# Kernel tuning notes

Hardware: AMD Instinct MI355X
Metric: run time of the kernel (lower is better)

## Reference

```python
import jax, jax.numpy as jnp
import numpy as np

HIDDEN = 1024
HEADS = 16
HEAD_D = HIDDEN // HEADS
FILL = -10000.0


def setup_inputs() -> dict:
    key = jax.random.key(0)
    ks = jax.random.split(key, 5)
    scale = 1.0 / np.sqrt(HIDDEN)
    x = jax.random.normal(ks[0], (2, 2048, HIDDEN), dtype=jnp.float32)
    # nn.Linear weights stored as [in, out] (already transposed vs torch)
    W_qkv = jax.random.uniform(ks[1], (HIDDEN, 3 * HIDDEN), dtype=jnp.float32, minval=-scale, maxval=scale)
    b_qkv = jax.random.uniform(ks[2], (3 * HIDDEN,), dtype=jnp.float32, minval=-scale, maxval=scale)
    W_o = jax.random.uniform(ks[3], (HIDDEN, HIDDEN), dtype=jnp.float32, minval=-scale, maxval=scale)
    b_o = jax.random.uniform(ks[4], (HIDDEN,), dtype=jnp.float32, minval=-scale, maxval=scale)
    return {"x": x, "W_qkv": W_qkv, "b_qkv": b_qkv, "W_o": W_o, "b_o": b_o}


def reference(x, W_qkv, b_qkv, W_o, b_o):
    b, s, _ = x.shape
    qkv = x @ W_qkv + b_qkv                       # [b, s, 3*hidden]
    q, k, v = jnp.split(qkv, 3, axis=-1)
    # [b, s, hidden] -> [b, h, s, d]
    def to_heads(t):
        return t.reshape(b, s, HEADS, HEAD_D).transpose(0, 2, 1, 3)
    q, k, v = to_heads(q), to_heads(k), to_heads(v)
    logits = jnp.einsum('bhqd,bhkd->bhqk', q, k) / np.sqrt(HEAD_D).astype(np.float32)
    # Faithful to the original: tril, then fill anything equal to 0 (incl.
    # genuine zeros) with the masked_logit_fill value.
    logits_tril = jnp.tril(logits)
    logits_masked = jnp.where(logits_tril == 0.0, jnp.float32(FILL), logits_tril)
    probs = jax.nn.softmax(logits_masked, axis=-1)
    pre_o = jnp.einsum('bhqk,bhkd->bhqd', probs, v)    # [b, h, s, d]
    pre_o = pre_o.transpose(0, 2, 1, 3).reshape(b, s, HIDDEN)
    return pre_o @ W_o + b_o
```

## Files before the change

### kernel.cpp

```cpp
#include <hip/hip_runtime.h>

typedef __attribute__((ext_vector_type(8))) short short8;
typedef __attribute__((ext_vector_type(4))) short short4b;
typedef __attribute__((ext_vector_type(4))) float f32x4;

static __device__ __forceinline__ short f2bf(float f) {
    unsigned u = __builtin_bit_cast(unsigned, f);
    u += 0x7FFFu + ((u >> 16) & 1u);
    return (short)(u >> 16);
}

static __device__ __forceinline__ void g2l16(const void* g, void* l) {
    __builtin_amdgcn_global_load_lds(
        (const __attribute__((address_space(1))) unsigned*)g,
        (__attribute__((address_space(3))) unsigned*)l, 16, 0, 0);
}

__global__ void convert_x(const float* __restrict__ x, short* __restrict__ xb, int n4) {
    int i = blockIdx.x * blockDim.x + threadIdx.x;
    if (i >= n4) return;
    f32x4 v = *(const f32x4*)&x[(long)i * 4];
    short4b o;
    #pragma unroll
    for (int j = 0; j < 4; ++j) o[j] = f2bf(v[j]);
    *(short4b*)&xb[(long)i * 4] = o;
}

__global__ void transpose_conv(const float* __restrict__ W, short* __restrict__ Wt,
                               int K, int N) {
    __shared__ float lds[64][65];
    const int t = threadIdx.x;
    const int n0 = blockIdx.x * 64, k0 = blockIdx.y * 64;
    const int rr = t >> 4, q4 = (t & 15) * 4;
    #pragma unroll
    for (int p = 0; p < 4; ++p) {
        int k = rr + p * 16;
        f32x4 v = *(const f32x4*)&W[(long)(k0 + k) * N + n0 + q4];
        #pragma unroll
        for (int j = 0; j < 4; ++j) lds[k][q4 + j] = v[j];
    }
    __syncthreads();
    #pragma unroll
    for (int p = 0; p < 4; ++p) {
        int nloc = rr + p * 16;
        short4b o;
        #pragma unroll
        for (int j = 0; j < 4; ++j) o[j] = f2bf(lds[q4 + j][nloc]);
        *(short4b*)&Wt[(long)(n0 + nloc) * K + k0 + q4] = o;
    }
}

template<int F32OUT>
__global__ __launch_bounds__(256, 2)
void gemm_bt(const short* __restrict__ A, const short* __restrict__ Bt,
             const float* __restrict__ bias, void* __restrict__ C,
             int M, int N, int K) {
    __shared__ short lA[128 * 32];
    __shared__ short lB[128 * 32];
    const int t = threadIdx.x;
    const int lane = t & 63, w = t >> 6;
    const int m0 = blockIdx.y * 128, n0 = blockIdx.x * 128;
    const int lr = lane & 15, lk = lane >> 4;
    const int wr = w >> 1, wc = w & 1;

    f32x4 acc[4][4];
    #pragma unroll
    for (int i = 0; i < 4; ++i)
        #pragma unroll
        for (int j = 0; j < 4; ++j)
            #pragma unroll
            for (int e = 0; e < 4; ++e) acc[i][j][e] = 0.0f;

    const int nsteps = K >> 5;
    for (int kt = 0; kt < nsteps; ++kt) {
        const int kb = kt * 32;
        #pragma unroll
        for (int c = 0; c < 2; ++c) {
            int off  = c * 4096 + w * 1024;
            int offl = off + lane * 16;
            int ra = offl >> 6;
            int ca = (offl & 63) >> 1;
            g2l16(A  + (long)(m0 + ra) * K + kb + ca, (short*)lA + (off >> 1));
            g2l16(Bt + (long)(n0 + ra) * K + kb + ca, (short*)lB + (off >> 1));
        }
        __syncthreads();
        short8 af[4], bf[4];
        #pragma unroll
        for (int m = 0; m < 4; ++m)
            af[m] = *(const short8*)&lA[(wr * 64 + m * 16 + lr) * 32 + lk * 8];
        #pragma unroll
        for (int n = 0; n < 4; ++n)
            bf[n] = *(const short8*)&lB[(wc * 64 + n * 16 + lr) * 32 + lk * 8];
        #pragma unroll
        for (int m = 0; m < 4; ++m)
            #pragma unroll
            for (int n = 0; n < 4; ++n)
                acc[m][n] = __builtin_amdgcn_mfma_f32_16x16x32_bf16(af[m], bf[n], acc[m][n], 0, 0, 0);
        __syncthreads();
    }

    #pragma unroll
    for (int n = 0; n < 4; ++n) {
        int col = n0 + wc * 64 + n * 16 + lr;
        float bb = bias[col];
        #pragma unroll
        for (int m = 0; m < 4; ++m) {
            int rowb = m0 + wr * 64 + m * 16 + lk * 4;
            #pragma unroll
            for (int r = 0; r < 4; ++r) {
                float v = acc[m][n][r] + bb;
                if (F32OUT) ((float*)C)[(long)(rowb + r) * N + col] = v;
                else        ((short*)C)[(long)(rowb + r) * N + col] = f2bf(v);
            }
        }
    }
}

__global__ void build_vt(const short* __restrict__ qkv, short* __restrict__ vt) {
    __shared__ short lds[64][72];
    const int t = threadIdx.x;
    const int st = blockIdx.x, bh = blockIdx.y;
    const int b = bh >> 4, h = bh & 15;
    const int s0 = st * 64;
    const int sr = t >> 3, c8 = (t & 7) * 8;
    #pragma unroll
    for (int p = 0; p < 2; ++p) {
        int s = sr + p * 32;
        short8 v = *(const short8*)&qkv[(long)(b * 2048 + s0 + s) * 3072 + 2048 + h * 64 + c8];
        *(short8*)&lds[s][c8] = v;
    }
    __syncthreads();
    #pragma unroll
    for (int p = 0; p < 2; ++p) {
        int d = sr + p * 32;
        short8 v;
        #pragma unroll
        for (int j = 0; j < 8; ++j) v[j] = lds[c8 + j][d];
        *(short8*)&vt[(long)(bh * 64 + d) * 2048 + s0 + c8] = v;
    }
}

__global__ __launch_bounds__(256, 2)
void attn_kernel(const short* __restrict__ qkv, const short* __restrict__ vt,
                 short* __restrict__ pre_o) {
    __shared__ short lK[64 * 64];
    __shared__ short lV[64 * 64];
    __shared__ short lP[4][32 * 64];
    const int t = threadIdx.x, lane = t & 63, w = t >> 6;
    const int lr = lane & 15, lk = lane >> 4;
    const int qt = blockIdx.x, bh = blockIdx.y;
    const int b = bh >> 4, h = bh & 15;
    const int q0 = qt * 128;

    short8 aq[2][2];
    #pragma unroll
    for (int m = 0; m < 2; ++m)
        #pragma unroll
        for (int dk = 0; dk < 2; ++dk)
            aq[m][dk] = *(const short8*)&qkv[(long)(b * 2048 + q0 + w * 32 + m * 16 + lr) * 3072
                                             + h * 64 + dk * 32 + lk * 8];

    f32x4 accO[2][4];
    #pragma unroll
    for (int m = 0; m < 2; ++m)
        #pragma unroll
        for (int n = 0; n < 4; ++n)
            #pragma unroll
            for (int e = 0; e < 4; ++e) accO[m][n][e] = 0.0f;
    float mst[2][4], lst[2][4];
    #pragma unroll
    for (int m = 0; m < 2; ++m)
        #pragma unroll
        for (int r = 0; r < 4; ++r) { mst[m][r] = -1e30f; lst[m][r] = 0.0f; }

    const int ntiles = 2 * qt + 2;
    for (int kt = 0; kt < ntiles; ++kt) {
        #pragma unroll
        for (int c = 0; c < 2; ++c) {
            int off   = c * 4096 + w * 1024;
            int offl  = off + lane * 16;
            int r     = offl >> 7;
            int slog  = ((offl >> 4) & 7) ^ (r & 7);
            g2l16(qkv + (long)(b * 2048 + kt * 64 + r) * 3072 + 1024 + h * 64 + slog * 8,
                  (short*)lK + (off >> 1));
            g2l16(vt + (long)(bh * 64 + r) * 2048 + kt * 64 + slog * 8,
                  (short*)lV + (off >> 1));
        }
        __syncthreads();

        f32x4 accS[2][4];
        #pragma unroll
        for (int m = 0; m < 2; ++m)
            #pragma unroll
            for (int n = 0; n < 4; ++n)
                #pragma unroll
                for (int e = 0; e < 4; ++e) accS[m][n][e] = 0.0f;
        short8 bk[4][2];
        #pragma unroll
        for (int n = 0; n < 4; ++n)
            #pragma unroll
            for (int dk = 0; dk < 2; ++dk)
                bk[n][dk] = *(const short8*)((const char*)lK + (n * 16 + lr) * 128
                                             + (((dk * 4 + lk) ^ (lr & 7)) << 4));
        #pragma unroll
        for (int m = 0; m < 2; ++m)
            #pragma unroll
            for (int n = 0; n < 4; ++n)
                #pragma unroll
                for (int dk = 0; dk < 2; ++dk)
                    accS[m][n] = __builtin_amdgcn_mfma_f32_16x16x32_bf16(aq[m][dk], bk[n][dk], accS[m][n], 0, 0, 0);

        #pragma unroll
        for (int m = 0; m < 2; ++m) {
            #pragma unroll
            for (int r = 0; r < 4; ++r) {
                int qrow = q0 + w * 32 + m * 16 + lk * 4 + r;
                float sv[4];
                float mx = -1e30f;
                #pragma unroll
                for (int n = 0; n < 4; ++n) {
                    float s = accS[m][n][r] * 0.125f;
                    int key = kt * 64 + n * 16 + lr;
                    if (key > qrow || s == 0.0f) s = -10000.0f;
                    sv[n] = s;
                    mx = fmaxf(mx, s);
                }
                mx = fmaxf(mx, __shfl_xor(mx, 1));
                mx = fmaxf(mx, __shfl_xor(mx, 2));
                mx = fmaxf(mx, __shfl_xor(mx, 4));
                mx = fmaxf(mx, __shfl_xor(mx, 8));
                float mnew = fmaxf(mst[m][r], mx);
                float corr = __expf(mst[m][r] - mnew);
                mst[m][r] = mnew;
                float rs = 0.0f;
                #pragma unroll
                for (int n = 0; n < 4; ++n) { float p = __expf(sv[n] - mnew); sv[n] = p; rs += p; }
                rs += __shfl_xor(rs, 1);
                rs += __shfl_xor(rs, 2);
                rs += __shfl_xor(rs, 4);
                rs += __shfl_xor(rs, 8);
                lst[m][r] = lst[m][r] * corr + rs;
                #pragma unroll
                for (int n = 0; n < 4; ++n) accO[m][n][r] *= corr;
                int pr = m * 16 + lk * 4 + r;
                int swz = (pr & 7) << 4;
                #pragma unroll
                for (int n = 0; n < 4; ++n) {
                    int pc = n * 16 + lr;
                    *(short*)((char*)&lP[w][0] + pr * 128 + ((pc * 2) ^ swz)) = f2bf(sv[n]);
                }
            }
        }

        short8 ap[2][2], bv[4][2];
        #pragma unroll
        for (int m = 0; m < 2; ++m)
            #pragma unroll
            for (int kk = 0; kk < 2; ++kk)
                ap[m][kk] = *(const short8*)((const char*)&lP[w][0] + (m * 16 + lr) * 128
                                             + (((kk * 4 + lk) ^ (lr & 7)) << 4));
        #pragma unroll
        for (int n = 0; n < 4; ++n)
            #pragma unroll
            for (int kk = 0; kk < 2; ++kk)
                bv[n][kk] = *(const short8*)((const char*)lV + (n * 16 + lr) * 128
                                             + (((kk * 4 + lk) ^ (lr & 7)) << 4));
        #pragma unroll
        for (int m = 0; m < 2; ++m)
            #pragma unroll
            for (int n = 0; n < 4; ++n)
                #pragma unroll
                for (int kk = 0; kk < 2; ++kk)
                    accO[m][n] = __builtin_amdgcn_mfma_f32_16x16x32_bf16(ap[m][kk], bv[n][kk], accO[m][n], 0, 0, 0);
        __syncthreads();
    }

    #pragma unroll
    for (int m = 0; m < 2; ++m) {
        #pragma unroll
        for (int r = 0; r < 4; ++r) {
            int qrow = q0 + w * 32 + m * 16 + lk * 4 + r;
            float inv = 1.0f / lst[m][r];
            #pragma unroll
            for (int n = 0; n < 4; ++n)
                pre_o[(long)(b * 2048 + qrow) * 1024 + h * 64 + n * 16 + lr] =
                    f2bf(accO[m][n][r] * inv);
        }
    }
}

extern "C" void kernel_launch(void* const* d_in, const int* in_sizes, int n_in,
                              void* d_out, int out_size, void* d_ws, size_t ws_size,
                              hipStream_t stream) {
    const float* x    = (const float*)d_in[0];
    const float* Wqkv = (const float*)d_in[1];
    const float* bqkv = (const float*)d_in[2];
    const float* Wo   = (const float*)d_in[3];
    const float* bo   = (const float*)d_in[4];
    float* out = (float*)d_out;

    char* ws = (char*)d_ws;
    short* xb    = (short*)(ws);
    short* wqkvT = (short*)(ws + (8L  << 20));
    short* woT   = (short*)(ws + (14L << 20));
    short* qkv   = (short*)(ws + (16L << 20));
    short* vt    = (short*)(ws + (40L << 20));
    short* preo  = (short*)(ws + (48L << 20));

    convert_x<<<4096, 256, 0, stream>>>(x, xb, 4096 * 1024 / 4);
    transpose_conv<<<dim3(48, 16), 256, 0, stream>>>(Wqkv, wqkvT, 1024, 3072);
    transpose_conv<<<dim3(16, 16), 256, 0, stream>>>(Wo, woT, 1024, 1024);
    gemm_bt<0><<<dim3(24, 32), 256, 0, stream>>>(xb, wqkvT, bqkv, qkv, 4096, 3072, 1024);
    build_vt<<<dim3(32, 32), 256, 0, stream>>>(qkv, vt);
    attn_kernel<<<dim3(16, 32), 256, 0, stream>>>(qkv, vt, preo);
    gemm_bt<1><<<dim3(8, 32), 256, 0, stream>>>(preo, woT, bo, out, 4096, 1024, 1024);
}
```

Before: 269.9 us.

## Double-buffer K/V tiles and pair causal query tiles per attention block

The attention kernel now double-buffers K and V tiles in LDS, issuing asynchronous global-to-LDS loads for the next key tile while the current one is computed. This is meant to hide the load latency that previously sat behind a barrier on every iteration. Each block also processes two 64-row query tiles, one from the start of the sequence and one from the end (pidx and 31-pidx), so every block does the same amount of causal work. The trade-off is twice the K/V LDS footprint and less MFMA work per wave per iteration, since each wave now handles 16 query rows instead of 32.

```diff
diff --git a/kernel.cpp b/kernel.cpp
--- a/kernel.cpp
+++ b/kernel.cpp
@@ -143,83 +143,95 @@
 __global__ __launch_bounds__(256, 2)
 void attn_kernel(const short* __restrict__ qkv, const short* __restrict__ vt,
                  short* __restrict__ pre_o) {
-    __shared__ short lK[64 * 64];
-    __shared__ short lV[64 * 64];
-    __shared__ short lP[4][32 * 64];
+    __shared__ short lK[2][64 * 64];
+    __shared__ short lV[2][64 * 64];
+    __shared__ short lP[4][16 * 64];
     const int t = threadIdx.x, lane = t & 63, w = t >> 6;
     const int lr = lane & 15, lk = lane >> 4;
-    const int qt = blockIdx.x, bh = blockIdx.y;
+    const int pidx = blockIdx.x, bh = blockIdx.y;
     const int b = bh >> 4, h = bh & 15;
-    const int q0 = qt * 128;
-
-    short8 aq[2][2];
-    #pragma unroll
-    for (int m = 0; m < 2; ++m)
+
+    int soff[2], sK_row[2], sslot[2];
+    #pragma unroll
+    for (int c = 0; c < 2; ++c) {
+        int off  = c * 4096 + w * 1024;
+        int offl = off + lane * 16;
+        int r    = offl >> 7;
+        soff[c]  = off >> 1;
+        sK_row[c] = r;
+        sslot[c] = (((offl >> 4) & 7) ^ (r & 7)) * 8;
+    }
+
+    #pragma unroll 1
+    for (int seg = 0; seg < 2; ++seg) {
+        const int Q  = seg ? (31 - pidx) : pidx;
+        const int q0 = Q * 64;
+        const int nt = seg ? (32 - pidx) : (pidx + 1);
+
+        short8 aq[2];
         #pragma unroll
         for (int dk = 0; dk < 2; ++dk)
-            aq[m][dk] = *(const short8*)&qkv[(long)(b * 2048 + q0 + w * 32 + m * 16 + lr) * 3072
-                                             + h * 64 + dk * 32 + lk * 8];
-
-    f32x4 accO[2][4];
-    #pragma unroll
-    for (int m = 0; m < 2; ++m)
+            aq[dk] = *(const short8*)&qkv[(long)(b * 2048 + q0 + w * 16 + lr) * 3072
+                                          + h * 64 + dk * 32 + lk * 8];
+
+        f32x4 accO[4];
         #pragma unroll
         for (int n = 0; n < 4; ++n)
             #pragma unroll
-            for (int e = 0; e < 4; ++e) accO[m][n][e] = 0.0f;
-    float mst[2][4], lst[2][4];
-    #pragma unroll
-    for (int m = 0; m < 2; ++m)
-        #pragma unroll
-        for (int r = 0; r < 4; ++r) { mst[m][r] = -1e30f; lst[m][r] = 0.0f; }
-
-    const int ntiles = 2 * qt + 2;
-    for (int kt = 0; kt < ntiles; ++kt) {
+            for (int e = 0; e < 4; ++e) accO[n][e] = 0.0f;
+        float mst[4], lst[4];
+        #pragma unroll
+        for (int r = 0; r < 4; ++r) { mst[r] = -1e30f; lst[r] = 0.0f; }
+
         #pragma unroll
         for (int c = 0; c < 2; ++c) {
-            int off   = c * 4096 + w * 1024;
-            int offl  = off + lane * 16;
-            int r     = offl >> 7;
-            int slog  = ((offl >> 4) & 7) ^ (r & 7);
-            g2l16(qkv + (long)(b * 2048 + kt * 64 + r) * 3072 + 1024 + h * 64 + slog * 8,
-                  (short*)lK + (off >> 1));
-            g2l16(vt + (long)(bh * 64 + r) * 2048 + kt * 64 + slog * 8,
-                  (short*)lV + (off >> 1));
+            g2l16(qkv + (long)(b * 2048 + 0 * 64 + sK_row[c]) * 3072 + 1024 + h * 64 + sslot[c],
+                  &lK[0][soff[c]]);
+            g2l16(vt + (long)(bh * 64 + sK_row[c]) * 2048 + 0 * 64 + sslot[c],
+                  &lV[0][soff[c]]);
         }
         __syncthreads();
 
-        f32x4 accS[2][4];
-        #pragma unroll
-        for (int m = 0; m < 2; ++m)
-            #pragma unroll
-            for (int n = 0; n < 4; ++n)
-                #pragma unroll
-                for (int e = 0; e < 4; ++e) accS[m][n][e] = 0.0f;
-        short8 bk[4][2];
-        #pragma unroll
-        for (int n = 0; n < 4; ++n)
-            #pragma unroll
-            for (int dk = 0; dk < 2; ++dk)
-                bk[n][dk] = *(const short8*)((const char*)lK + (n * 16 + lr) * 128
-                                             + (((dk * 4 + lk) ^ (lr & 7)) << 4));
-        #pragma unroll
-        for (int m = 0; m < 2; ++m)
+        #pragma unroll 1
+        for (int kt = 0; kt < nt; ++kt) {
+            const int cur = kt & 1;
+            if (kt + 1 < nt) {
+                #pragma unroll
+                for (int c = 0; c < 2; ++c) {
+                    g2l16(qkv + (long)(b * 2048 + (kt + 1) * 64 + sK_row[c]) * 3072
+                              + 1024 + h * 64 + sslot[c],
+                          &lK[cur ^ 1][soff[c]]);
+                    g2l16(vt + (long)(bh * 64 + sK_row[c]) * 2048 + (kt + 1) * 64 + sslot[c],
+                          &lV[cur ^ 1][soff[c]]);
+                }
+            }
+
+            f32x4 accS[4];
+            #pragma unroll
+            for (int n = 0; n < 4; ++n)
+                #pragma unroll
+                for (int e = 0; e < 4; ++e) accS[n][e] = 0.0f;
+            short8 bk[4][2];
             #pragma unroll
             for (int n = 0; n < 4; ++n)
                 #pragma unroll
                 for (int dk = 0; dk < 2; ++dk)
-                    accS[m][n] = __builtin_amdgcn_mfma_f32_16x16x32_bf16(aq[m][dk], bk[n][dk], accS[m][n], 0, 0, 0);
-
-        #pragma unroll
-        for (int m = 0; m < 2; ++m) {
+                    bk[n][dk] = *(const short8*)((const char*)&lK[cur][0] + (n * 16 + lr) * 128
+                                                 + (((dk * 4 + lk) ^ (lr & 7)) << 4));
+            #pragma unroll
+            for (int n = 0; n < 4; ++n)
+                #pragma unroll
+                for (int dk = 0; dk < 2; ++dk)
+                    accS[n] = __builtin_amdgcn_mfma_f32_16x16x32_bf16(aq[dk], bk[n][dk], accS[n], 0, 0, 0);
+
             #pragma unroll
             for (int r = 0; r < 4; ++r) {
-                int qrow = q0 + w * 32 + m * 16 + lk * 4 + r;
+                int qrow = q0 + w * 16 + lk * 4 + r;
                 float sv[4];
                 float mx = -1e30f;
                 #pragma unroll
                 for (int n = 0; n < 4; ++n) {
-                    float s = accS[m][n][r] * 0.125f;
+                    float s = accS[n][r] * 0.125f;
                     int key = kt * 64 + n * 16 + lr;
                     if (key > qrow || s == 0.0f) s = -10000.0f;
                     sv[n] = s;
@@ -229,9 +241,9 @@
                 mx = fmaxf(mx, __shfl_xor(mx, 2));
                 mx = fmaxf(mx, __shfl_xor(mx, 4));
                 mx = fmaxf(mx, __shfl_xor(mx, 8));
-                float mnew = fmaxf(mst[m][r], mx);
-                float corr = __expf(mst[m][r] - mnew);
-                mst[m][r] = mnew;
+                float mnew = fmaxf(mst[r], mx);
+                float corr = __expf(mst[r] - mnew);
+                mst[r] = mnew;
                 float rs = 0.0f;
                 #pragma unroll
                 for (int n = 0; n < 4; ++n) { float p = __expf(sv[n] - mnew); sv[n] = p; rs += p; }
@@ -239,52 +251,46 @@
                 rs += __shfl_xor(rs, 2);
                 rs += __shfl_xor(rs, 4);
                 rs += __shfl_xor(rs, 8);
-                lst[m][r] = lst[m][r] * corr + rs;
-                #pragma unroll
-                for (int n = 0; n < 4; ++n) accO[m][n][r] *= corr;
-                int pr = m * 16 + lk * 4 + r;
-                int swz = (pr & 7) << 4;
+                lst[r] = lst[r] * corr + rs;
+                #pragma unroll
+                for (int n = 0; n < 4; ++n) accO[n][r] *= corr;
+                int prr = lk * 4 + r;
+                int swz = (prr & 7) << 4;
                 #pragma unroll
                 for (int n = 0; n < 4; ++n) {
                     int pc = n * 16 + lr;
-                    *(short*)((char*)&lP[w][0] + pr * 128 + ((pc * 2) ^ swz)) = f2bf(sv[n]);
+                    *(short*)((char*)&lP[w][0] + prr * 128 + ((pc * 2) ^ swz)) = f2bf(sv[n]);
                 }
             }
-        }
-
-        short8 ap[2][2], bv[4][2];
-        #pragma unroll
-        for (int m = 0; m < 2; ++m)
+
+            short8 ap[2], bv[4][2];
             #pragma unroll
             for (int kk = 0; kk < 2; ++kk)
-                ap[m][kk] = *(const short8*)((const char*)&lP[w][0] + (m * 16 + lr) * 128
-                                             + (((kk * 4 + lk) ^ (lr & 7)) << 4));
-        #pragma unroll
-        for (int n = 0; n < 4; ++n)
-            #pragma unroll
-            for (int kk = 0; kk < 2; ++kk)
-                bv[n][kk] = *(const short8*)((const char*)lV + (n * 16 + lr) * 128
-                                             + (((kk * 4 + lk) ^ (lr & 7)) << 4));
-        #pragma unroll
-        for (int m = 0; m < 2; ++m)
+                ap[kk] = *(const short8*)((const char*)&lP[w][0] + lr * 128
+                                          + (((kk * 4 + lk) ^ (lr & 7)) << 4));
             #pragma unroll
             for (int n = 0; n < 4; ++n)
                 #pragma unroll
                 for (int kk = 0; kk < 2; ++kk)
-                    accO[m][n] = __builtin_amdgcn_mfma_f32_16x16x32_bf16(ap[m][kk], bv[n][kk], accO[m][n], 0, 0, 0);
-        __syncthreads();
-    }
-
-    #pragma unroll
-    for (int m = 0; m < 2; ++m) {
+                    bv[n][kk] = *(const short8*)((const char*)&lV[cur][0] + (n * 16 + lr) * 128
+                                                 + (((kk * 4 + lk) ^ (lr & 7)) << 4));
+            #pragma unroll
+            for (int n = 0; n < 4; ++n)
+                #pragma unroll
+                for (int kk = 0; kk < 2; ++kk)
+                    accO[n] = __builtin_amdgcn_mfma_f32_16x16x32_bf16(ap[kk], bv[n][kk], accO[n], 0, 0, 0);
+
+            __syncthreads();
+        }
+
         #pragma unroll
         for (int r = 0; r < 4; ++r) {
-            int qrow = q0 + w * 32 + m * 16 + lk * 4 + r;
-            float inv = 1.0f / lst[m][r];
+            int qrow = q0 + w * 16 + lk * 4 + r;
+            float inv = 1.0f / lst[r];
             #pragma unroll
             for (int n = 0; n < 4; ++n)
                 pre_o[(long)(b * 2048 + qrow) * 1024 + h * 64 + n * 16 + lr] =
-                    f2bf(accO[m][n][r] * inv);
+                    f2bf(accO[n][r] * inv);
         }
     }
 }
```

Measured after the change: 224.6 us. 16.8% less time.
